# Kernel tuning notes

Measured on AMD Instinct MI355X. Metric: run time of the kernel, lower is better.

Reference implementation:

```python
import jax, jax.numpy as jnp
import numpy as np

H = 2048          # hidden_size
NH = 16           # num_attention_heads
HD = H // NH      # head_dim = 128
RD = HD // 2      # rotary dim = 64
LAT = H // 8      # latent_dim = 256
B, S = 2, 2048
BASE = 10000.0


def rotary_emb(seq_len, dtype=jnp.float32):
    # DeepseekRotaryEmbedding(dim=RD): inv_freq over arange(0, RD, 2)
    inv_freq = 1.0 / (BASE ** (np.arange(0, RD, 2, dtype=np.float32) / RD))  # [RD//2]
    pos = jnp.arange(seq_len, dtype=dtype)
    sincos = pos[:, None] * jnp.asarray(inv_freq, dtype)                     # [S, RD//2]
    return jnp.concatenate([jnp.sin(sincos), jnp.cos(sincos)], axis=-1)      # [S, RD]


def apply_rope(x, emb):
    # x: [B, S, NH, RD]; emb: [S, RD] with sin first half, cos second half
    half = RD // 2
    x1, x2 = x[..., :half], x[..., half:]
    sin = emb[:, None, :half]   # [S, 1, half] broadcast over heads
    cos = emb[:, None, half:]
    return jnp.concatenate([x1 * cos - x2 * sin, x1 * sin + x2 * cos], axis=-1)


def setup_inputs() -> dict:
    key = jax.random.key(0)
    ks = jax.random.split(key, 9)
    def w(k, shape):
        return jax.random.normal(k, shape, dtype=jnp.float32) * (1.0 / np.sqrt(shape[-1]))
    return {
        "hidden_states": jax.random.normal(ks[0], (B, S, H), dtype=jnp.float32),
        "W_kv_d": w(ks[1], (LAT, H)),
        "W_q_d": w(ks[2], (LAT, H)),
        "W_k_u": w(ks[3], (H // 2, LAT)),
        "W_q_u": w(ks[4], (H // 2, LAT)),
        "W_v_u": w(ks[5], (H, LAT)),
        "W_rope_k": w(ks[6], (H // 2, H)),
        "W_rope_q": w(ks[7], (H // 2, LAT)),
        "W_o": w(ks[8], (H, H)),
    }


def reference(hidden_states, W_kv_d, W_q_d, W_k_u, W_q_u, W_v_u, W_rope_k, W_rope_q, W_o):
    x = hidden_states                                   # [B, S, H]
    kv_d = x @ W_kv_d.T                                 # [B, S, LAT]
    q_d = x @ W_q_d.T                                   # [B, S, LAT]
    k_c = (kv_d @ W_k_u.T).reshape(B, S, NH, RD)        # content half of k
    q_c = (q_d @ W_q_u.T).reshape(B, S, NH, RD)
    v = (kv_d @ W_v_u.T).reshape(B, S, NH, HD)
    k_r = (x @ W_rope_k.T).reshape(B, S, NH, RD)
    q_r = (q_d @ W_rope_q.T).reshape(B, S, NH, RD)

    emb = rotary_emb(S, x.dtype)                        # [S, RD]
    q_r = apply_rope(q_r, emb)
    k_r = apply_rope(k_r, emb)

    q = jnp.concatenate([q_c, q_r], axis=-1)            # [B, S, NH, HD]
    k = jnp.concatenate([k_c, k_r], axis=-1)

    scale = 1.0 / np.sqrt(HD)                           # SDPA default scale
    scores = jnp.einsum("bqhd,bkhd->bhqk", q, k) * scale
    causal = jnp.tril(jnp.ones((S, S), dtype=bool))
    scores = jnp.where(causal, scores, jnp.finfo(scores.dtype).min)
    probs = jax.nn.softmax(scores, axis=-1)
    y = jnp.einsum("bhqk,bkhd->bqhd", probs, v).reshape(B, S, H)
    return y @ W_o.T
```

## Files before the change

kernel.cpp:

```cpp
#include <hip/hip_runtime.h>

typedef unsigned short u16;
typedef unsigned int u32;
typedef __attribute__((ext_vector_type(8))) short bf16x8;
typedef __attribute__((ext_vector_type(4))) float f32x4;

#define DEVI static __device__ __forceinline__

DEVI u16 f2b(float f){
  u32 x = __float_as_uint(f);
  return (u16)((x + 0x7fffu + ((x >> 16) & 1u)) >> 16);
}
DEVI float b2f(u16 u){ return __uint_as_float(((u32)u) << 16); }
DEVI float2 up2(u32 u){
  return make_float2(__uint_as_float(u << 16), __uint_as_float(u & 0xffff0000u));
}
DEVI void gload16(const u16* g, u16* l){
  __builtin_amdgcn_global_load_lds((const __attribute__((address_space(1))) void*)g,
                                   (__attribute__((address_space(3))) void*)l,
                                   16, 0, 0);
}

#define QSCALE 0.12751744900929456f

struct CSrc { const float* s[9]; };
__global__ void cvt_all(CSrc cs, u16* __restrict__ xb, u16* __restrict__ wcat){
  int i = blockIdx.x * 256 + threadIdx.x;
  if (i >= 4259840) return;
  const float4* s; int lo, di; uint2* d;
  if (i < 2097152){
    s = (const float4*)cs.s[0]; lo = 0; di = i; d = (uint2*)xb;
  } else {
    int j = i - 2097152; di = j; d = (uint2*)wcat;
    if      (j <  131072){ s = (const float4*)cs.s[1]; lo = 0;       }
    else if (j <  262144){ s = (const float4*)cs.s[2]; lo = 131072;  }
    else if (j <  786432){ s = (const float4*)cs.s[3]; lo = 262144;  }
    else if (j <  851968){ s = (const float4*)cs.s[4]; lo = 786432;  }
    else if (j <  917504){ s = (const float4*)cs.s[5]; lo = 851968;  }
    else if (j <  983040){ s = (const float4*)cs.s[6]; lo = 917504;  }
    else if (j < 1114112){ s = (const float4*)cs.s[7]; lo = 983040;  }
    else                 { s = (const float4*)cs.s[8]; lo = 1114112; }
  }
  float4 f = s[di - lo];
  u32 a = (u32)f2b(f.x) | ((u32)f2b(f.y) << 16);
  u32 b = (u32)f2b(f.z) | ((u32)f2b(f.w) << 16);
  d[di] = make_uint2(a, b);
}

template<int MODE>
__global__ __launch_bounds__(256, 2)
void gemm_bt(const u16* __restrict__ A, int lda, const u16* __restrict__ W,
             void* __restrict__ D, int N, int K){
  __shared__ u16 As[128 * 32];
  __shared__ u16 Bs[128 * 32];
  const int tid = threadIdx.x;
  const int wave = tid >> 6, lane = tid & 63;
  const int lr = lane & 15, lk = lane >> 4;
  int bid = blockIdx.y * gridDim.x + blockIdx.x;
  const int nwg = gridDim.x * gridDim.y;
  bid = (bid & 7) * (nwg >> 3) + (bid >> 3);
  const int bx = bid % gridDim.x, by = bid / gridDim.x;
  const int m0 = by * 128, n0 = bx * 128;
  const int wm = wave >> 1, wn = wave & 1;
  f32x4 acc[4][4] = {};

  const u16* a0 = A + (size_t)(m0 + (tid >> 2)) * lda + (tid & 3) * 8;
  const u16* a1 = a0 + (size_t)64 * lda;
  const u16* b0 = W + (size_t)(n0 + (tid >> 2)) * K + (tid & 3) * 8;
  const u16* b1 = b0 + (size_t)64 * K;
  u16* lA0 = As + wave * 512;  u16* lA1 = As + 2048 + wave * 512;
  u16* lB0 = Bs + wave * 512;  u16* lB1 = Bs + 2048 + wave * 512;

  for (int k0 = 0; k0 < K; k0 += 32){
    __syncthreads();
    gload16(a0 + k0, lA0);
    gload16(a1 + k0, lA1);
    gload16(b0 + k0, lB0);
    gload16(b1 + k0, lB1);
    asm volatile("s_waitcnt vmcnt(0)" ::: "memory");
    __syncthreads();
    bf16x8 af[4], bfr[4];
    #pragma unroll
    for (int i = 0; i < 4; i++)
      af[i] = *(const bf16x8*)(As + (wm * 64 + i * 16 + lr) * 32 + lk * 8);
    #pragma unroll
    for (int j = 0; j < 4; j++)
      bfr[j] = *(const bf16x8*)(Bs + (wn * 64 + j * 16 + lr) * 32 + lk * 8);
    #pragma unroll
    for (int i = 0; i < 4; i++)
      #pragma unroll
      for (int j = 0; j < 4; j++)
        acc[i][j] = __builtin_amdgcn_mfma_f32_16x16x32_bf16(af[i], bfr[j], acc[i][j], 0, 0, 0);
  }

  const int rb = (lane >> 4) * 4, cl = lane & 15;
  #pragma unroll
  for (int i = 0; i < 4; i++){
    #pragma unroll
    for (int j = 0; j < 4; j++){
      const int mb = m0 + wm * 64 + i * 16 + rb;
      const int n  = n0 + wn * 64 + j * 16 + cl;
      #pragma unroll
      for (int r = 0; r < 4; r++){
        int m = mb + r;
        float v = acc[i][j][r];
        if (MODE == 0) ((u16*)D)[(size_t)m * N + n] = f2b(v);
        else           ((float*)D)[(size_t)m * N + n] = v;
      }
    }
  }
}

__global__ __launch_bounds__(256, 2)
void gemm_up(const u16* __restrict__ dcat, const u16* __restrict__ qW,
             const u16* __restrict__ kvW, u16* __restrict__ qbuf,
             u16* __restrict__ qrp, u16* __restrict__ kbuf, u16* __restrict__ vt){
  __shared__ u16 As[128 * 32];
  __shared__ u16 Bs[128 * 32];
  const int tid = threadIdx.x;
  const int wave = tid >> 6, lane = tid & 63;
  const int lr = lane & 15, lk = lane >> 4;
  int bid = blockIdx.y * 40 + blockIdx.x;
  bid = (bid & 7) * 160 + (bid >> 3);
  const int bx = bid % 40, by = bid / 40;
  const bool qside = bx < 16;
  const u16* A = qside ? dcat + 256 : dcat;
  const u16* W = qside ? qW : kvW;
  const int n0 = (qside ? bx : bx - 16) * 128;
  const int m0 = by * 128;
  const int wm = wave >> 1, wn = wave & 1;
  f32x4 acc[4][4] = {};

  const u16* a0 = A + (size_t)(m0 + (tid >> 2)) * 1536 + (tid & 3) * 8;
  const u16* a1 = a0 + (size_t)64 * 1536;
  const u16* b0 = W + (size_t)(n0 + (tid >> 2)) * 256 + (tid & 3) * 8;
  const u16* b1 = b0 + (size_t)64 * 256;
  u16* lA0 = As + wave * 512;  u16* lA1 = As + 2048 + wave * 512;
  u16* lB0 = Bs + wave * 512;  u16* lB1 = Bs + 2048 + wave * 512;

  for (int k0 = 0; k0 < 256; k0 += 32){
    __syncthreads();
    gload16(a0 + k0, lA0);
    gload16(a1 + k0, lA1);
    gload16(b0 + k0, lB0);
    gload16(b1 + k0, lB1);
    asm volatile("s_waitcnt vmcnt(0)" ::: "memory");
    __syncthreads();
    bf16x8 af[4], bfr[4];
    #pragma unroll
    for (int i = 0; i < 4; i++)
      af[i] = *(const bf16x8*)(As + (wm * 64 + i * 16 + lr) * 32 + lk * 8);
    #pragma unroll
    for (int j = 0; j < 4; j++)
      bfr[j] = *(const bf16x8*)(Bs + (wn * 64 + j * 16 + lr) * 32 + lk * 8);
    #pragma unroll
    for (int i = 0; i < 4; i++)
      #pragma unroll
      for (int j = 0; j < 4; j++)
        acc[i][j] = __builtin_amdgcn_mfma_f32_16x16x32_bf16(af[i], bfr[j], acc[i][j], 0, 0, 0);
  }

  const int rb = (lane >> 4) * 4, cl = lane & 15;
  #pragma unroll
  for (int i = 0; i < 4; i++){
    #pragma unroll
    for (int j = 0; j < 4; j++){
      const int mb = m0 + wm * 64 + i * 16 + rb;
      const int n  = n0 + wn * 64 + j * 16 + cl;
      if (!qside && n >= 1024){
        int n1 = n - 1024, h = n1 >> 7, d = n1 & 127, b = mb >> 11, s = mb & 2047;
        u32 lo = (u32)f2b(acc[i][j][0]) | ((u32)f2b(acc[i][j][1]) << 16);
        u32 hi = (u32)f2b(acc[i][j][2]) | ((u32)f2b(acc[i][j][3]) << 16);
        *(uint2*)(vt + (((size_t)(b * 16 + h) * 128 + d) * 2048 + s)) = make_uint2(lo, hi);
      } else {
        #pragma unroll
        for (int r = 0; r < 4; r++){
          int m = mb + r;
          float v = acc[i][j][r];
          if (qside){
            if (n < 1024){
              qrp[(size_t)m * 1024 + n] = f2b(v);
            } else {
              int n1 = n - 1024, h = n1 >> 6, d = n1 & 63;
              qbuf[(((size_t)(m >> 11) * 16 + h) * 2048 + (m & 2047)) * 128 + d] = f2b(v * QSCALE);
            }
          } else {
            int h = n >> 6, d = n & 63;
            kbuf[(((size_t)(m >> 11) * 16 + h) * 2048 + (m & 2047)) * 128 + d] = f2b(v);
          }
        }
      }
    }
  }
}

__global__ void rope_k(const u16* __restrict__ qrp, const u16* __restrict__ dcat,
                       u16* __restrict__ Qb, u16* __restrict__ Kb){
  int idx = blockIdx.x * 256 + threadIdx.x;
  if (idx >= (1 << 21)) return;
  int j = idx & 31, h = (idx >> 5) & 15, s = (idx >> 9) & 2047, b = (idx >> 20) & 1;
  float inv = exp2f((float)j * (-13.287712379549449f / 32.0f));
  float ang = (float)s * inv;
  float sn = sinf(ang), cs = cosf(ang);
  size_t soq = ((size_t)(b * 2048 + s)) * 1024 + h * 64 + j;
  size_t sok = ((size_t)(b * 2048 + s)) * 1536 + 512 + h * 64 + j;
  size_t dd = (((size_t)(b * 16 + h)) * 2048 + s) * 128;
  {
    float x1 = b2f(qrp[soq]), x2 = b2f(qrp[soq + 32]);
    Qb[dd + 64 + j] = f2b((x1 * cs - x2 * sn) * QSCALE);
    Qb[dd + 96 + j] = f2b((x1 * sn + x2 * cs) * QSCALE);
  }
  {
    float x1 = b2f(dcat[sok]), x2 = b2f(dcat[sok + 32]);
    Kb[dd + 64 + j] = f2b(x1 * cs - x2 * sn);
    Kb[dd + 96 + j] = f2b(x1 * sn + x2 * cs);
  }
}

__global__ __launch_bounds__(512, 1)
void flash_part(const u16* __restrict__ Q, const u16* __restrict__ K,
                const u16* __restrict__ VT, u16* __restrict__ Op0,
                u16* __restrict__ Op1, float2* __restrict__ ML){
  __shared__ u16 k_s[3][8192];
  __shared__ u16 v_s[8192];
  __shared__ u16 p_s[8][2048];
  const int tid = threadIdx.x;
  const int w = tid >> 6, l = tid & 63;
  const int lr = l & 15, hk = l >> 4;
  const int bh = blockIdx.x;
  const int qt = 7 - blockIdx.y;
  const int z  = blockIdx.z;
  const int b = bh >> 4, h = bh & 15;
  const size_t base = (size_t)bh * 2048 * 128;
  const u16* Qb = Q + base;
  const u16* Kb = K + base;
  const u16* Vb = VT + base;
  u16* myp = p_s[w];
  const int q0 = qt * 256 + w * 32;
  const int T  = 2 * qt + 2;
  const int t0 = z * T;

  bf16x8 qa[2][4];
  #pragma unroll
  for (int mi = 0; mi < 2; mi++)
    #pragma unroll
    for (int ks = 0; ks < 4; ks++)
      qa[mi][ks] = *(const bf16x8*)(Qb + (size_t)(q0 + mi * 16 + lr) * 128 + ks * 32 + hk * 8);

  f32x4 o[2][8] = {};
  float mbase[2] = {-1e30f, -1e30f};
  float lsum[2] = {0.f, 0.f};

  auto STAGE_K = [&](int kt, int buf){
    #pragma unroll
    for (int it = 0; it < 2; ++it){
      int row = it * 32 + w * 4 + (l >> 4);
      gload16(Kb + (size_t)(kt * 64 + row) * 128 + (((l & 15) ^ (row & 15)) << 3),
              &k_s[buf][it * 4096 + w * 512]);
    }
  };
  auto STAGE_V = [&](int kt){
    #pragma unroll
    for (int it = 0; it < 2; ++it){
      int d = it * 64 + w * 8 + (l >> 3);
      gload16(Vb + (size_t)d * 2048 + kt * 64 + (((l & 7) ^ (d & 7)) << 3),
              &v_s[it * 4096 + w * 512]);
    }
  };

  STAGE_K(t0, 0);
  STAGE_K(t0 + 1, 1);
  asm volatile("s_waitcnt vmcnt(2)" ::: "memory");
  __builtin_amdgcn_s_barrier();

  for (int tt = 0; tt < T; ++tt){
    const int t = t0 + tt;
    STAGE_V(t);
    const bool pre2 = (tt + 2 < T);
    if (pre2) STAGE_K(t + 2, (tt + 2) % 3);

    const bool act = (t * 64 <= q0 + 31);
    if (act){
      const u16* ks_ = k_s[tt % 3];
      f32x4 sc[2][4] = {};
      #pragma unroll
      for (int ksd = 0; ksd < 4; ++ksd){
        bf16x8 kb[4];
        #pragma unroll
        for (int nj = 0; nj < 4; ++nj){
          int row = nj * 16 + lr;
          kb[nj] = *(const bf16x8*)(ks_ + row * 128 + (((ksd * 4 + hk) ^ lr) << 3));
        }
        __builtin_amdgcn_s_setprio(1);
        #pragma unroll
        for (int mi = 0; mi < 2; ++mi)
          #pragma unroll
          for (int nj = 0; nj < 4; ++nj)
            sc[mi][nj] = __builtin_amdgcn_mfma_f32_16x16x32_bf16(kb[nj], qa[mi][ksd], sc[mi][nj], 0, 0, 0);
        __builtin_amdgcn_s_setprio(0);
      }
      float lmax[2] = {-3e38f, -3e38f};
      if (t * 64 + 63 > q0){
        #pragma unroll
        for (int mi = 0; mi < 2; ++mi){
          int qrow = q0 + mi * 16 + lr;
          #pragma unroll
          for (int nj = 0; nj < 4; ++nj)
            #pragma unroll
            for (int r = 0; r < 4; ++r){
              int kc = t * 64 + nj * 16 + hk * 4 + r;
              float s = (kc <= qrow) ? sc[mi][nj][r] : -1e30f;
              sc[mi][nj][r] = s;
              lmax[mi] = fmaxf(lmax[mi], s);
            }
        }
      } else {
        #pragma unroll
        for (int mi = 0; mi < 2; ++mi)
          #pragma unroll
          for (int nj = 0; nj < 4; ++nj)
            #pragma unroll
            for (int r = 0; r < 4; ++r)
              lmax[mi] = fmaxf(lmax[mi], sc[mi][nj][r]);
      }
      #pragma unroll
      for (int mi = 0; mi < 2; ++mi){
        float mx = lmax[mi];
        mx = fmaxf(mx, __shfl_xor(mx, 16));
        mx = fmaxf(mx, __shfl_xor(mx, 32));
        float mnew = fmaxf(mbase[mi], mx);
        float alpha = exp2f(mbase[mi] - mnew);
        mbase[mi] = mnew;
        lsum[mi] *= alpha;
        #pragma unroll
        for (int dj = 0; dj < 8; ++dj)
          #pragma unroll
          for (int r = 0; r < 4; ++r) o[mi][dj][r] *= alpha;
      }
      #pragma unroll
      for (int mi = 0; mi < 2; ++mi){
        u16* prow = myp + (mi * 16 + lr) * 64;
        float rs = 0.f;
        #pragma unroll
        for (int nj = 0; nj < 4; ++nj){
          float p0 = exp2f(sc[mi][nj][0] - mbase[mi]);
          float p1 = exp2f(sc[mi][nj][1] - mbase[mi]);
          float p2 = exp2f(sc[mi][nj][2] - mbase[mi]);
          float p3 = exp2f(sc[mi][nj][3] - mbase[mi]);
          rs += (p0 + p1) + (p2 + p3);
          u32 a = (u32)f2b(p0) | ((u32)f2b(p1) << 16);
          u32 c = (u32)f2b(p2) | ((u32)f2b(p3) << 16);
          *(uint2*)(prow + ((nj * 16 + hk * 4) ^ ((lr & 7) << 3))) = make_uint2(a, c);
        }
        lsum[mi] += rs;
      }
    }

    if (pre2) asm volatile("s_waitcnt vmcnt(2)" ::: "memory");
    else      asm volatile("s_waitcnt vmcnt(0)" ::: "memory");
    __builtin_amdgcn_s_barrier();
    asm volatile("s_waitcnt lgkmcnt(0)" ::: "memory");
    __builtin_amdgcn_sched_barrier(0);

    if (act){
      #pragma unroll
      for (int kk = 0; kk < 2; ++kk){
        bf16x8 pb[2], va[8];
        #pragma unroll
        for (int mi = 0; mi < 2; ++mi)
          pb[mi] = *(const bf16x8*)(myp + (mi * 16 + lr) * 64 +
                     ((kk * 32 + hk * 8) ^ ((lr & 7) << 3)));
        #pragma unroll
        for (int dj = 0; dj < 8; ++dj){
          int d = dj * 16 + lr;
          va[dj] = *(const bf16x8*)(&v_s[d * 64 + (((kk * 4 + hk) ^ (lr & 7)) << 3)]);
        }
        __builtin_amdgcn_s_setprio(1);
        #pragma unroll
        for (int mi = 0; mi < 2; ++mi)
          #pragma unroll
          for (int dj = 0; dj < 8; ++dj)
            o[mi][dj] = __builtin_amdgcn_mfma_f32_16x16x32_bf16(va[dj], pb[mi], o[mi][dj], 0, 0, 0);
        __builtin_amdgcn_s_setprio(0);
      }
    }

    __builtin_amdgcn_s_barrier();
  }

  u16* Op = z ? Op1 : Op0;
  u16* scr = myp;
  #pragma unroll
  for (int mi = 0; mi < 2; ++mi){
    float lt = lsum[mi];
    lt += __shfl_xor(lt, 16);
    lt += __shfl_xor(lt, 32);
    if (hk == 0){
      float2 v; v.x = mbase[mi]; v.y = lt;
      ML[((size_t)z * 32 + bh) * 2048 + qt * 256 + w * 32 + mi * 16 + lr] = v;
    }
    #pragma unroll
    for (int dj = 0; dj < 8; ++dj){
      u32 a = (u32)f2b(o[mi][dj][0]) | ((u32)f2b(o[mi][dj][1]) << 16);
      u32 c = (u32)f2b(o[mi][dj][2]) | ((u32)f2b(o[mi][dj][3]) << 16);
      *(uint2*)(scr + lr * 128 + ((dj * 16 + hk * 4) ^ ((lr & 7) << 3))) = make_uint2(a, c);
    }
    asm volatile("s_waitcnt lgkmcnt(0)" ::: "memory");
    __builtin_amdgcn_sched_barrier(0);
    #pragma unroll
    for (int rr = 0; rr < 4; ++rr){
      int row = rr * 4 + hk;
      uint4 vv = *(const uint4*)(scr + row * 128 + ((lr * 8) ^ ((row & 7) << 3)));
      *(uint4*)(Op + ((size_t)(b * 2048) + qt * 256 + w * 32 + mi * 16 + row) * 2048
                    + h * 128 + lr * 8) = vv;
    }
    asm volatile("s_waitcnt lgkmcnt(0)" ::: "memory");
    __builtin_amdgcn_sched_barrier(0);
  }
}

__global__ void merge_k(const u16* __restrict__ Op0, const u16* __restrict__ Op1,
                        const float2* __restrict__ ML, u16* __restrict__ Y){
  int i = blockIdx.x * 256 + threadIdx.x;
  if (i >= (1 << 20)) return;
  int row = i >> 8;
  int c8 = (i & 255) << 3;
  int b = row >> 11, s = row & 2047, h = c8 >> 7;
  int bh = b * 16 + h;
  float2 ml0 = ML[(size_t)bh * 2048 + s];
  float2 ml1 = ML[(size_t)(32 + bh) * 2048 + s];
  float m = fmaxf(ml0.x, ml1.x);
  float w0 = exp2f(ml0.x - m), w1 = exp2f(ml1.x - m);
  float inv = 1.0f / fmaxf(ml0.y * w0 + ml1.y * w1, 1e-30f);
  size_t off = (size_t)row * 2048 + c8;
  uint4 a = *(const uint4*)(Op0 + off);
  uint4 c = *(const uint4*)(Op1 + off);
  u32 res[4];
  u32 au[4] = {a.x, a.y, a.z, a.w};
  u32 cu[4] = {c.x, c.y, c.z, c.w};
  #pragma unroll
  for (int j = 0; j < 4; ++j){
    float2 f = up2(au[j]), g = up2(cu[j]);
    float r0 = (f.x * w0 + g.x * w1) * inv;
    float r1 = (f.y * w0 + g.y * w1) * inv;
    res[j] = (u32)f2b(r0) | ((u32)f2b(r1) << 16);
  }
  *(uint4*)(Y + off) = make_uint4(res[0], res[1], res[2], res[3]);
}

extern "C" void kernel_launch(void* const* d_in, const int* in_sizes, int n_in,
                              void* d_out, int out_size, void* d_ws, size_t ws_size,
                              hipStream_t stream){
  u16* p = (u16*)d_ws;
  auto alloc = [&](size_t n){ u16* r = p; p += n; return r; };
  u16* wcat = alloc(8650752);
  u16* downW  = wcat;
  u16* qcatW  = wcat + 3145728;
  u16* kvcatW = wcat + 3670016;
  u16* wo     = wcat + 4456448;
  u16* xb   = alloc(8388608);
  u16* dcat = alloc(6291456);
  u16* qrp  = alloc(4194304);
  u16* qbuf = alloc(8388608);
  u16* kbuf = alloc(8388608);
  u16* vt   = alloc(8388608);
  u16* ybuf = alloc(8388608);
  float2* ml = (float2*)alloc(524288);

  CSrc cs;
  cs.s[0] = (const float*)d_in[0];
  cs.s[1] = (const float*)d_in[1];
  cs.s[2] = (const float*)d_in[2];
  cs.s[3] = (const float*)d_in[6];
  cs.s[4] = (const float*)d_in[7];
  cs.s[5] = (const float*)d_in[4];
  cs.s[6] = (const float*)d_in[3];
  cs.s[7] = (const float*)d_in[5];
  cs.s[8] = (const float*)d_in[8];
  cvt_all<<<16640, 256, 0, stream>>>(cs, xb, wcat);

  dim3 blk(256);
  gemm_bt<0><<<dim3(12, 32), blk, 0, stream>>>(xb, 2048, downW, dcat, 1536, 2048);
  gemm_up<<<dim3(40, 32), blk, 0, stream>>>(dcat, qcatW, kvcatW, qbuf, qrp, kbuf, vt);
  rope_k<<<(1 << 21) / 256, 256, 0, stream>>>(qrp, dcat, qbuf, kbuf);
  u16* op0 = xb;
  u16* op1 = dcat;
  flash_part<<<dim3(32, 8, 2), dim3(512), 0, stream>>>(qbuf, kbuf, vt, op0, op1, ml);
  merge_k<<<4096, 256, 0, stream>>>(op0, op1, ml, ybuf);
  gemm_bt<3><<<dim3(16, 32), blk, 0, stream>>>(ybuf, 2048, wo, d_out, 2048, 2048);
}
```

Before: 218.1 us.

## Replace down/output GEMMs with 256x128 triple-buffered swizzled-LDS pipelined kernel

The simple single-stage 128x128 GEMM used for the down projection and output projection is replaced by a 512-thread kernel with 256x128 tiles and K-step 64. LDS is triple-buffered, with async global-to-LDS loads for tile t+2 issued during compute on tile t. An XOR swizzle is added to avoid LDS bank conflicts, and setprio is raised around the MFMA bursts. The aim is to hide memory latency and raise operand reuse. In exchange it uses much more LDS (about 144KB), runs one block per CU, and launches fewer blocks (192 and 256), which may leave some CUs idle.

```diff
diff --git a/kernel.cpp b/kernel.cpp
--- a/kernel.cpp
+++ b/kernel.cpp
@@ -48,61 +48,98 @@
 }
 
 template<int MODE>
-__global__ __launch_bounds__(256, 2)
-void gemm_bt(const u16* __restrict__ A, int lda, const u16* __restrict__ W,
-             void* __restrict__ D, int N, int K){
-  __shared__ u16 As[128 * 32];
-  __shared__ u16 Bs[128 * 32];
+__global__ __launch_bounds__(512, 1)
+void gemm_big(const u16* __restrict__ A, int lda, const u16* __restrict__ W,
+              void* __restrict__ D, int N, int K){
+  __shared__ u16 A_s[3][256 * 64];
+  __shared__ u16 B_s[3][128 * 64];
   const int tid = threadIdx.x;
-  const int wave = tid >> 6, lane = tid & 63;
-  const int lr = lane & 15, lk = lane >> 4;
+  const int w = tid >> 6, l = tid & 63;
+  const int lr = l & 15, hk = l >> 4;
+  const int wm = w >> 1, wn = w & 1;
   int bid = blockIdx.y * gridDim.x + blockIdx.x;
   const int nwg = gridDim.x * gridDim.y;
   bid = (bid & 7) * (nwg >> 3) + (bid >> 3);
   const int bx = bid % gridDim.x, by = bid / gridDim.x;
-  const int m0 = by * 128, n0 = bx * 128;
-  const int wm = wave >> 1, wn = wave & 1;
+  const int m0 = by * 256, n0 = bx * 128;
+  const int nt = K >> 6;
   f32x4 acc[4][4] = {};
 
-  const u16* a0 = A + (size_t)(m0 + (tid >> 2)) * lda + (tid & 3) * 8;
-  const u16* a1 = a0 + (size_t)64 * lda;
-  const u16* b0 = W + (size_t)(n0 + (tid >> 2)) * K + (tid & 3) * 8;
-  const u16* b1 = b0 + (size_t)64 * K;
-  u16* lA0 = As + wave * 512;  u16* lA1 = As + 2048 + wave * 512;
-  u16* lB0 = Bs + wave * 512;  u16* lB1 = Bs + 2048 + wave * 512;
-
-  for (int k0 = 0; k0 < K; k0 += 32){
-    __syncthreads();
-    gload16(a0 + k0, lA0);
-    gload16(a1 + k0, lA1);
-    gload16(b0 + k0, lB0);
-    gload16(b1 + k0, lB1);
-    asm volatile("s_waitcnt vmcnt(0)" ::: "memory");
-    __syncthreads();
-    bf16x8 af[4], bfr[4];
-    #pragma unroll
-    for (int i = 0; i < 4; i++)
-      af[i] = *(const bf16x8*)(As + (wm * 64 + i * 16 + lr) * 32 + lk * 8);
-    #pragma unroll
-    for (int j = 0; j < 4; j++)
-      bfr[j] = *(const bf16x8*)(Bs + (wn * 64 + j * 16 + lr) * 32 + lk * 8);
-    #pragma unroll
-    for (int i = 0; i < 4; i++)
-      #pragma unroll
-      for (int j = 0; j < 4; j++)
-        acc[i][j] = __builtin_amdgcn_mfma_f32_16x16x32_bf16(af[i], bfr[j], acc[i][j], 0, 0, 0);
-  }
-
-  const int rb = (lane >> 4) * 4, cl = lane & 15;
+  auto STAGE_A = [&](int t, int s){
+    int row = s * 64 + w * 8 + (l >> 3);
+    gload16(A + (size_t)(m0 + row) * lda + t * 64 + (((l & 7) ^ (row & 7)) << 3),
+            &A_s[t % 3][s * 4096 + w * 512]);
+  };
+  auto STAGE_B = [&](int t, int s){
+    int row = s * 64 + w * 8 + (l >> 3);
+    gload16(W + (size_t)(n0 + row) * K + t * 64 + (((l & 7) ^ (row & 7)) << 3),
+            &B_s[t % 3][s * 4096 + w * 512]);
+  };
+  auto STAGE_ALL = [&](int t){
+    STAGE_A(t, 0); STAGE_A(t, 1); STAGE_A(t, 2); STAGE_A(t, 3);
+    STAGE_B(t, 0); STAGE_B(t, 1);
+  };
+
+  STAGE_ALL(0);
+  STAGE_ALL(1);
+  asm volatile("s_waitcnt vmcnt(6)" ::: "memory");
+  __builtin_amdgcn_s_barrier();
+
+  for (int t = 0; t < nt; ++t){
+    const bool pre2 = (t + 2 < nt);
+    const u16* As_ = A_s[t % 3];
+    const u16* Bs_ = B_s[t % 3];
+    #pragma unroll
+    for (int ph = 0; ph < 4; ++ph){
+      const int mq = ph >> 1, nq = ph & 1;
+      bf16x8 af[2][2], bf[2][2];
+      #pragma unroll
+      for (int i = 0; i < 2; ++i){
+        int row = wm * 64 + (2 * mq + i) * 16 + lr;
+        int rowb = wn * 64 + (2 * nq + i) * 16 + lr;
+        #pragma unroll
+        for (int kk = 0; kk < 2; ++kk){
+          af[i][kk] = *(const bf16x8*)(As_ + row * 64 + (((kk * 4 + hk) ^ (row & 7)) << 3));
+          bf[i][kk] = *(const bf16x8*)(Bs_ + rowb * 64 + (((kk * 4 + hk) ^ (rowb & 7)) << 3));
+        }
+      }
+      if (pre2){
+        if (ph == 0){ STAGE_A(t + 2, 0); STAGE_A(t + 2, 1); }
+        else if (ph == 1){ STAGE_A(t + 2, 2); STAGE_A(t + 2, 3); }
+        else if (ph == 2){ STAGE_B(t + 2, 0); }
+        else            { STAGE_B(t + 2, 1); }
+      }
+      __builtin_amdgcn_s_barrier();
+      asm volatile("s_waitcnt lgkmcnt(0)" ::: "memory");
+      __builtin_amdgcn_sched_barrier(0);
+      __builtin_amdgcn_s_setprio(1);
+      #pragma unroll
+      for (int i = 0; i < 2; ++i)
+        #pragma unroll
+        for (int j = 0; j < 2; ++j)
+          #pragma unroll
+          for (int kk = 0; kk < 2; ++kk)
+            acc[2 * mq + i][2 * nq + j] =
+              __builtin_amdgcn_mfma_f32_16x16x32_bf16(af[i][kk], bf[j][kk],
+                                                      acc[2 * mq + i][2 * nq + j], 0, 0, 0);
+      __builtin_amdgcn_s_setprio(0);
+      if (ph == 3 && t + 1 < nt){
+        if (pre2) asm volatile("s_waitcnt vmcnt(6)" ::: "memory");
+        else      asm volatile("s_waitcnt vmcnt(0)" ::: "memory");
+      }
+      __builtin_amdgcn_s_barrier();
+    }
+  }
+
+  const int rb = (l >> 4) * 4, cl = l & 15;
   #pragma unroll
-  for (int i = 0; i < 4; i++){
-    #pragma unroll
-    for (int j = 0; j < 4; j++){
-      const int mb = m0 + wm * 64 + i * 16 + rb;
-      const int n  = n0 + wn * 64 + j * 16 + cl;
-      #pragma unroll
-      for (int r = 0; r < 4; r++){
-        int m = mb + r;
+  for (int i = 0; i < 4; ++i){
+    #pragma unroll
+    for (int j = 0; j < 4; ++j){
+      #pragma unroll
+      for (int r = 0; r < 4; ++r){
+        int m = m0 + wm * 64 + i * 16 + rb + r;
+        int n = n0 + wn * 64 + j * 16 + cl;
         float v = acc[i][j][r];
         if (MODE == 0) ((u16*)D)[(size_t)m * N + n] = f2b(v);
         else           ((float*)D)[(size_t)m * N + n] = v;
@@ -479,13 +516,12 @@
   cs.s[8] = (const float*)d_in[8];
   cvt_all<<<16640, 256, 0, stream>>>(cs, xb, wcat);
 
-  dim3 blk(256);
-  gemm_bt<0><<<dim3(12, 32), blk, 0, stream>>>(xb, 2048, downW, dcat, 1536, 2048);
-  gemm_up<<<dim3(40, 32), blk, 0, stream>>>(dcat, qcatW, kvcatW, qbuf, qrp, kbuf, vt);
+  gemm_big<0><<<dim3(12, 16), dim3(512), 0, stream>>>(xb, 2048, downW, dcat, 1536, 2048);
+  gemm_up<<<dim3(40, 32), dim3(256), 0, stream>>>(dcat, qcatW, kvcatW, qbuf, qrp, kbuf, vt);
   rope_k<<<(1 << 21) / 256, 256, 0, stream>>>(qrp, dcat, qbuf, kbuf);
   u16* op0 = xb;
   u16* op1 = dcat;
   flash_part<<<dim3(32, 8, 2), dim3(512), 0, stream>>>(qbuf, kbuf, vt, op0, op1, ml);
   merge_k<<<4096, 256, 0, stream>>>(op0, op1, ml, ybuf);
-  gemm_bt<3><<<dim3(16, 32), blk, 0, stream>>>(ybuf, 2048, wo, d_out, 2048, 2048);
-}
+  gemm_big<3><<<dim3(16, 16), dim3(512), 0, stream>>>(ybuf, 2048, wo, d_out, 2048, 2048);
+}
```

Measured after the change: 235.0 us. +7.7%, slower.
